# Kernel optimization log

Hardware: AMD Instinct MI355X
Metric: run time of the kernel (lower is better)

## Reference

```python
import jax, jax.numpy as jnp
import numpy as np

ATTN_MULT = 8.0
NEG_INF = float('-inf')

N, Q, S, D = 16, 2048, 2048, 64


def setup_inputs() -> dict:
    key = jax.random.key(0)
    kq, kk, kv, kp = jax.random.split(key, 4)
    return {
        "queries_nqd": jax.random.normal(kq, (N, Q, D), dtype=jnp.float32),
        "keys_nsd": jax.random.normal(kk, (N, S, D), dtype=jnp.float32),
        "values_nsv": jax.random.normal(kv, (N, S, D), dtype=jnp.float32),
        "prefix_len_n": jax.random.randint(kp, (N,), 0, S, dtype=jnp.int64 if jax.config.jax_enable_x64 else jnp.int32),
    }


def reference(queries_nqd, keys_nsd, values_nsv, prefix_len_n):
    # attention_type == 'block_diagonal', backend == 'torch', dropout p == 0
    n, q, d = queries_nqd.shape
    s = keys_nsd.shape[1]
    scale = ATTN_MULT / d
    # prefix-block mask: key position < prefix_len (broadcast over queries)
    block_mask_n1s = (jnp.arange(s)[None, None, :] < prefix_len_n[:, None, None])  # [n,1,s]
    diag_mask_qs = jnp.arange(q)[:, None] == jnp.arange(s)[None, :]                # [q,s]
    mask_nqs = block_mask_n1s | diag_mask_qs[None, :, :]                           # [n,q,s]
    scores_nqs = jnp.einsum('nqd,nsd->nqs', queries_nqd, keys_nsd) * scale
    scores_nqs = jnp.where(mask_nqs, scores_nqs, NEG_INF)
    probs_nqs = jax.nn.softmax(scores_nqs, axis=-1)
    return jnp.einsum('nqs,nsv->nqv', probs_nqs, values_nsv)
```

## Files before the change

kernel.cpp:

```cpp
#include <hip/hip_runtime.h>
#include <hip/hip_bf16.h>
#include <math.h>

#define NH 16
#define QL 2048
#define SL 2048
#define DD 64
#define BQ 128
#define NSPLIT 2
#define SPL 1024
#define NTILE 16
#define PSTR 72
#define QK_SCALE_LOG2E 0.1803368801111f

typedef __attribute__((ext_vector_type(8))) short short8;
typedef __attribute__((ext_vector_type(4))) float floatx4;
typedef __attribute__((ext_vector_type(4))) unsigned short ushort4v;
typedef __attribute__((ext_vector_type(8))) unsigned short ushort8v;

__device__ __forceinline__ unsigned short f2bf(float x) {
    unsigned u = __float_as_uint(x);
    u += 0x7FFFu + ((u >> 16) & 1u);
    return (unsigned short)(u >> 16);
}
__device__ __forceinline__ unsigned int f2bf2u(float x, float y) {
    __hip_bfloat162 h = __float22bfloat162_rn(make_float2(x, y));
    return *(unsigned int*)&h;
}
__device__ __forceinline__ float bf2f(unsigned short h) {
    return __uint_as_float((unsigned)h << 16);
}

__device__ __forceinline__ void gld16(const unsigned short* g, unsigned short* l) {
    __builtin_amdgcn_global_load_lds(
        (const __attribute__((address_space(1))) unsigned int*)g,
        (__attribute__((address_space(3))) unsigned int*)l, 16, 0, 0);
}

__global__ __launch_bounds__(512) void k_prep(
    const float* __restrict__ Kf, const float* __restrict__ Vf,
    unsigned short* __restrict__ Kb, unsigned short* __restrict__ Vtb)
{
    __shared__ unsigned short sT[64][PSTR];
    const int bx = (int)blockIdx.x, tid = (int)threadIdx.x;

    const int gidx = bx * 512 + tid;
    #pragma unroll
    for (int k = 0; k < 2; ++k) {
        int idx = gidx + k * (512 * 512);
        float4 v = ((const float4*)Kf)[idx];
        ushort4v h = { f2bf(v.x), f2bf(v.y), f2bf(v.z), f2bf(v.w) };
        *(ushort4v*)(Kb + (size_t)idx * 4) = h;
    }

    const int n = bx >> 5, s0 = (bx & 31) * 64;
    const float* vb = Vf + ((size_t)n * SL + s0) * DD;
    #pragma unroll
    for (int i = 0; i < 2; ++i) {
        int idx = tid + i * 512;
        int r = idx >> 4, c = (idx & 15) << 2;
        float4 v = *(const float4*)(vb + r * DD + c);
        sT[c + 0][r] = f2bf(v.x);
        sT[c + 1][r] = f2bf(v.y);
        sT[c + 2][r] = f2bf(v.z);
        sT[c + 3][r] = f2bf(v.w);
    }
    __syncthreads();
    const int d = tid >> 3, sg = tid & 7;
    unsigned short* out = Vtb + (size_t)n * DD * SL + (size_t)d * SL + s0 + sg * 8;
    ushort8v a;
    #pragma unroll
    for (int i = 0; i < 8; ++i) a[i] = sT[d][sg * 8 + i];
    *(ushort8v*)out = a;
}

__global__ __launch_bounds__(512, 6) void k_attn(
    const float* __restrict__ Qf, const unsigned short* __restrict__ Kb,
    const unsigned short* __restrict__ Vtb, const int* __restrict__ plen_g,
    unsigned short* __restrict__ Opb, float* __restrict__ Lp)
{
    __shared__ unsigned short sK[2][64 * 64];
    __shared__ unsigned short sVt[2][64 * 64];
    __shared__ unsigned short sP[8 * 16 * 64];

    const int flat = (int)blockIdx.x;
    const int sp   = flat >> 8;
    const int rb   = flat & 255;
    const int n    = (rb + sp) & (NH - 1);
    const int qt   = rb >> 4;
    const int q0   = qt * BQ;
    const int sbeg = sp * SPL;
    const int plen = plen_g[n];
    const bool hasdiag = (q0 >= sbeg) && (q0 < sbeg + SPL);
    if (!((sbeg < plen) || hasdiag)) return;

    const int tid  = (int)threadIdx.x;
    const int wave = tid >> 6, lane = tid & 63, quad = lane >> 4, l16 = lane & 15;

    int rem  = plen - sbeg;
    int base = (rem > 0) ? min((rem + 63) >> 6, NTILE) : 0;
    int td0 = -1, td1 = -1;
    if (hasdiag) {
        int d0 = (q0 - sbeg) >> 6;
        if (d0 >= base) td0 = d0;
        if (d0 + 1 >= base) td1 = d0 + 1;
    }
    const int total = base + (td0 >= 0) + (td1 >= 0);

    const int qrow  = wave * 16 + l16;
    const int qglob = q0 + qrow;
    const int pmask = (l16 & 7) * 8;

    const unsigned short* kh = Kb  + (size_t)n * SL * DD;
    const unsigned short* vh = Vtb + (size_t)n * DD * SL;

    const int srow = wave * 8 + (lane >> 3);
    const int scol = ((lane & 7) ^ (srow & 7)) * 8;

    auto tile_of = [&](int i) -> int {
        if (i < base) return i;
        if (i == base) return (td0 >= 0) ? td0 : td1;
        return td1;
    };

    {
        int t0 = tile_of(0);
        const unsigned short* kg = kh + (size_t)(sbeg + t0 * 64) * DD;
        const unsigned short* vg = vh + (sbeg + t0 * 64);
        gld16(kg + srow * DD + scol, sK[0] + wave * 512);
        gld16(vg + (size_t)srow * SL + scol, sVt[0] + wave * 512);
    }

    short8 bQ0, bQ1;
    {
        const float* qf = Qf + ((size_t)(n * QL + qglob)) * DD + quad * 8;
        float4 a0 = *(const float4*)(qf);
        float4 a1 = *(const float4*)(qf + 4);
        float4 c0 = *(const float4*)(qf + 32);
        float4 c1 = *(const float4*)(qf + 36);
        const float S = QK_SCALE_LOG2E;
        unsigned int u0[4] = {
            f2bf2u(a0.x * S, a0.y * S), f2bf2u(a0.z * S, a0.w * S),
            f2bf2u(a1.x * S, a1.y * S), f2bf2u(a1.z * S, a1.w * S) };
        unsigned int u1[4] = {
            f2bf2u(c0.x * S, c0.y * S), f2bf2u(c0.z * S, c0.w * S),
            f2bf2u(c1.x * S, c1.y * S), f2bf2u(c1.z * S, c1.w * S) };
        bQ0 = *(short8*)u0;
        bQ1 = *(short8*)u1;
    }

    floatx4 acc[4];
    #pragma unroll
    for (int dt = 0; dt < 4; ++dt) acc[dt] = (floatx4){0.f, 0.f, 0.f, 0.f};
    float lsum = 0.f;
    unsigned short* pw = sP + qrow * 64;

    for (int i = 0; i < total; ++i) {
        __syncthreads();

        if (i + 1 < total) {
            int tn = tile_of(i + 1);
            const unsigned short* kg = kh + (size_t)(sbeg + tn * 64) * DD;
            const unsigned short* vg = vh + (sbeg + tn * 64);
            gld16(kg + srow * DD + scol, sK[(i + 1) & 1] + wave * 512);
            gld16(vg + (size_t)srow * SL + scol, sVt[(i + 1) & 1] + wave * 512);
        }

        const unsigned short* sk = sK[i & 1];
        const unsigned short* sv = sVt[i & 1];
        const int t  = tile_of(i);
        const int s0 = sbeg + t * 64;

        floatx4 sf[4];
        #pragma unroll
        for (int st2 = 0; st2 < 4; ++st2) sf[st2] = (floatx4){0.f, 0.f, 0.f, 0.f};
        __builtin_amdgcn_s_setprio(1);
        #pragma unroll
        for (int st2 = 0; st2 < 4; ++st2) {
            int krow = st2 * 16 + l16;
            short8 aK0 = *(const short8*)(sk + krow * 64 + (((0 * 4 + quad) ^ (krow & 7)) * 8));
            short8 aK1 = *(const short8*)(sk + krow * 64 + (((1 * 4 + quad) ^ (krow & 7)) * 8));
            sf[st2] = __builtin_amdgcn_mfma_f32_16x16x32_bf16(aK0, bQ0, sf[st2], 0, 0, 0);
            sf[st2] = __builtin_amdgcn_mfma_f32_16x16x32_bf16(aK1, bQ1, sf[st2], 0, 0, 0);
        }
        __builtin_amdgcn_s_setprio(0);

        if (s0 + 64 <= plen) {
            #pragma unroll
            for (int st2 = 0; st2 < 4; ++st2) {
                float p0 = __builtin_amdgcn_exp2f(sf[st2][0]);
                float p1 = __builtin_amdgcn_exp2f(sf[st2][1]);
                float p2 = __builtin_amdgcn_exp2f(sf[st2][2]);
                float p3 = __builtin_amdgcn_exp2f(sf[st2][3]);
                lsum += (p0 + p1) + (p2 + p3);
                uint2 pk = { f2bf2u(p0, p1), f2bf2u(p2, p3) };
                *(uint2*)(pw + ((st2 * 16 + quad * 4) ^ pmask)) = pk;
            }
        } else {
            #pragma unroll
            for (int st2 = 0; st2 < 4; ++st2) {
                float p[4];
                #pragma unroll
                for (int r2 = 0; r2 < 4; ++r2) {
                    int s = s0 + st2 * 16 + quad * 4 + r2;
                    bool valid = (s < plen) || (s == qglob);
                    p[r2] = __builtin_amdgcn_exp2f(valid ? sf[st2][r2] : -INFINITY);
                    lsum += p[r2];
                }
                uint2 pk = { f2bf2u(p[0], p[1]), f2bf2u(p[2], p[3]) };
                *(uint2*)(pw + ((st2 * 16 + quad * 4) ^ pmask)) = pk;
            }
        }

        __builtin_amdgcn_s_setprio(1);
        #pragma unroll
        for (int ks = 0; ks < 2; ++ks) {
            short8 aP = *(const short8*)(pw + ((ks * 32 + quad * 8) ^ pmask));
            #pragma unroll
            for (int dt = 0; dt < 4; ++dt) {
                int vrow = dt * 16 + l16;
                short8 bV = *(const short8*)(sv + vrow * 64 + (((ks * 4 + quad) ^ (vrow & 7)) * 8));
                acc[dt] = __builtin_amdgcn_mfma_f32_16x16x32_bf16(aP, bV, acc[dt], 0, 0, 0);
            }
        }
        __builtin_amdgcn_s_setprio(0);
    }

    lsum += __shfl_xor(lsum, 16, 64);
    lsum += __shfl_xor(lsum, 32, 64);
    if (quad == 0)
        Lp[((size_t)sp * NH + n) * QL + q0 + qrow] = lsum;

    unsigned short* pws = sP + wave * 16 * 64;
    #pragma unroll
    for (int dt = 0; dt < 4; ++dt) {
        int chunk = dt * 2 + (l16 >> 3);
        #pragma unroll
        for (int r2 = 0; r2 < 4; ++r2) {
            int row = quad * 4 + r2;
            int sw = ((chunk ^ (row & 7)) * 8) + (l16 & 7);
            pws[row * 64 + sw] = f2bf(acc[dt][r2]);
        }
    }
    const size_t qbase = ((size_t)sp * NH + n) * QL + q0 + wave * 16;
    #pragma unroll
    for (int t2 = 0; t2 < 2; ++t2) {
        int row = t2 * 8 + (lane >> 3);
        int chunk = lane & 7;
        int sw = (chunk ^ (row & 7)) * 8;
        ushort8v val = *(const ushort8v*)(pws + row * 64 + sw);
        *(ushort8v*)(Opb + (qbase + row) * DD + chunk * 8) = val;
    }
}

__global__ __launch_bounds__(512) void k_combine(
    const unsigned short* __restrict__ Opb, const float* __restrict__ Lp,
    const int* __restrict__ plen_g, float* __restrict__ Og)
{
    const int idx = (int)(blockIdx.x * 512 + threadIdx.x);
    const int d8 = idx & 7;
    const int q  = (idx >> 3) & (QL - 1);
    const int n  = idx >> 14;
    const int plen = plen_g[n];
    const int spd = q >> 10;
    float s[8];
    #pragma unroll
    for (int j = 0; j < 8; ++j) s[j] = 0.f;
    float l = 0.f;
    #pragma unroll
    for (int sp = 0; sp < NSPLIT; ++sp) {
        if ((sp * SPL < plen) || (sp == spd)) {
            const unsigned short* ob = Opb + (((size_t)sp * NH + n) * QL + q) * DD + d8 * 8;
            ushort8v v = *(const ushort8v*)ob;
            #pragma unroll
            for (int j = 0; j < 8; ++j) s[j] += bf2f(v[j]);
            l += Lp[((size_t)sp * NH + n) * QL + q];
        }
    }
    const float inv = 1.0f / l;
    float4 o0 = { s[0] * inv, s[1] * inv, s[2] * inv, s[3] * inv };
    float4 o1 = { s[4] * inv, s[5] * inv, s[6] * inv, s[7] * inv };
    float* og = Og + ((size_t)n * QL + q) * DD + d8 * 8;
    *(float4*)og = o0;
    *(float4*)(og + 4) = o1;
}

extern "C" void kernel_launch(void* const* d_in, const int* in_sizes, int n_in,
                              void* d_out, int out_size, void* d_ws, size_t ws_size,
                              hipStream_t stream) {
    const float* Qf   = (const float*)d_in[0];
    const float* Kf   = (const float*)d_in[1];
    const float* Vf   = (const float*)d_in[2];
    const int*   plen = (const int*)d_in[3];
    float* Og = (float*)d_out;

    char* ws = (char*)d_ws;
    unsigned short* Kb  = (unsigned short*)(ws);
    unsigned short* Vtb = (unsigned short*)(ws + (4u << 20));
    unsigned short* Opb = (unsigned short*)(ws + (8u << 20));
    float*          Lp  = (float*)(ws + (16u << 20));

    k_prep<<<512, 512, 0, stream>>>(Kf, Vf, Kb, Vtb);
    k_attn<<<NSPLIT * 256, 512, 0, stream>>>(Qf, Kb, Vtb, plen, Opb, Lp);
    k_combine<<<512, 512, 0, stream>>>(Opb, Lp, plen, Og);
}
```

Measured before the change: 107.2 us.

## Interleave key tiles across splits and triple-buffer K/V loads with explicit waitcnt

The key sequence is now split between the two split-K blocks by tile parity (even tiles to one split, odd tiles to the other) instead of contiguous halves. This balances prefix work between the splits, since a short prefix previously loaded nearly all the work onto the first split. Each split also takes one of the two diagonal tiles, so both splits always produce output and the combine kernel drops its plen-dependent checks. The K/V shared-memory staging becomes a 3-deep ring with manual vmcnt waits and raw barriers, keeping two tiles in flight. The extra LDS this needs is why the occupancy hint drops from 6 to 4 blocks.

```diff
diff --git a/kernel.cpp b/kernel.cpp
--- a/kernel.cpp
+++ b/kernel.cpp
@@ -8,8 +8,6 @@
 #define DD 64
 #define BQ 128
 #define NSPLIT 2
-#define SPL 1024
-#define NTILE 16
 #define PSTR 72
 #define QK_SCALE_LOG2E 0.1803368801111f
 
@@ -74,13 +72,13 @@
     *(ushort8v*)out = a;
 }
 
-__global__ __launch_bounds__(512, 6) void k_attn(
+__global__ __launch_bounds__(512, 4) void k_attn(
     const float* __restrict__ Qf, const unsigned short* __restrict__ Kb,
     const unsigned short* __restrict__ Vtb, const int* __restrict__ plen_g,
     unsigned short* __restrict__ Opb, float* __restrict__ Lp)
 {
-    __shared__ unsigned short sK[2][64 * 64];
-    __shared__ unsigned short sVt[2][64 * 64];
+    __shared__ unsigned short sK[3][64 * 64];
+    __shared__ unsigned short sVt[3][64 * 64];
     __shared__ unsigned short sP[8 * 16 * 64];
 
     const int flat = (int)blockIdx.x;
@@ -89,23 +87,16 @@
     const int n    = (rb + sp) & (NH - 1);
     const int qt   = rb >> 4;
     const int q0   = qt * BQ;
-    const int sbeg = sp * SPL;
     const int plen = plen_g[n];
-    const bool hasdiag = (q0 >= sbeg) && (q0 < sbeg + SPL);
-    if (!((sbeg < plen) || hasdiag)) return;
 
     const int tid  = (int)threadIdx.x;
     const int wave = tid >> 6, lane = tid & 63, quad = lane >> 4, l16 = lane & 15;
 
-    int rem  = plen - sbeg;
-    int base = (rem > 0) ? min((rem + 63) >> 6, NTILE) : 0;
-    int td0 = -1, td1 = -1;
-    if (hasdiag) {
-        int d0 = (q0 - sbeg) >> 6;
-        if (d0 >= base) td0 = d0;
-        if (d0 + 1 >= base) td1 = d0 + 1;
-    }
-    const int total = base + (td0 >= 0) + (td1 >= 0);
+    const int ptiles = (plen + 63) >> 6;
+    const int d0     = q0 >> 6;
+    const int tdiag  = d0 + sp;
+    const int cnt_p  = (ptiles + 1 - sp) >> 1;
+    const int total  = cnt_p + (tdiag >= ptiles ? 1 : 0);
 
     const int qrow  = wave * 16 + l16;
     const int qglob = q0 + qrow;
@@ -118,18 +109,14 @@
     const int scol = ((lane & 7) ^ (srow & 7)) * 8;
 
     auto tile_of = [&](int i) -> int {
-        if (i < base) return i;
-        if (i == base) return (td0 >= 0) ? td0 : td1;
-        return td1;
+        return (i < cnt_p) ? (sp + (i << 1)) : tdiag;
     };
-
-    {
-        int t0 = tile_of(0);
-        const unsigned short* kg = kh + (size_t)(sbeg + t0 * 64) * DD;
-        const unsigned short* vg = vh + (sbeg + t0 * 64);
-        gld16(kg + srow * DD + scol, sK[0] + wave * 512);
-        gld16(vg + (size_t)srow * SL + scol, sVt[0] + wave * 512);
-    }
+    auto stage = [&](int t, int b) {
+        const unsigned short* kg = kh + ((size_t)t << 6) * DD;
+        const unsigned short* vg = vh + (t << 6);
+        gld16(kg + srow * DD + scol, sK[b] + wave * 512);
+        gld16(vg + (size_t)srow * SL + scol, sVt[b] + wave * 512);
+    };
 
     short8 bQ0, bQ1;
     {
@@ -149,27 +136,31 @@
         bQ1 = *(short8*)u1;
     }
 
+    stage(tile_of(0), 0);
+    if (total > 1) stage(tile_of(1), 1);
+
     floatx4 acc[4];
     #pragma unroll
     for (int dt = 0; dt < 4; ++dt) acc[dt] = (floatx4){0.f, 0.f, 0.f, 0.f};
     float lsum = 0.f;
     unsigned short* pw = sP + qrow * 64;
 
+    int bi = 0;
+    int bs = 2;
     for (int i = 0; i < total; ++i) {
-        __syncthreads();
-
-        if (i + 1 < total) {
-            int tn = tile_of(i + 1);
-            const unsigned short* kg = kh + (size_t)(sbeg + tn * 64) * DD;
-            const unsigned short* vg = vh + (sbeg + tn * 64);
-            gld16(kg + srow * DD + scol, sK[(i + 1) & 1] + wave * 512);
-            gld16(vg + (size_t)srow * SL + scol, sVt[(i + 1) & 1] + wave * 512);
-        }
-
-        const unsigned short* sk = sK[i & 1];
-        const unsigned short* sv = sVt[i & 1];
+        if (i + 2 <= total) {
+            asm volatile("s_waitcnt vmcnt(2) lgkmcnt(0)" ::: "memory");
+        } else {
+            asm volatile("s_waitcnt vmcnt(0) lgkmcnt(0)" ::: "memory");
+        }
+        __builtin_amdgcn_s_barrier();
+
+        if (i + 2 < total) stage(tile_of(i + 2), bs);
+
+        const unsigned short* sk = sK[bi];
+        const unsigned short* sv = sVt[bi];
         const int t  = tile_of(i);
-        const int s0 = sbeg + t * 64;
+        const int s0 = t << 6;
 
         floatx4 sf[4];
         #pragma unroll
@@ -224,6 +215,9 @@
             }
         }
         __builtin_amdgcn_s_setprio(0);
+
+        bi = (bi == 2) ? 0 : bi + 1;
+        bs = (bs == 2) ? 0 : bs + 1;
     }
 
     lsum += __shfl_xor(lsum, 16, 64);
@@ -255,27 +249,23 @@
 
 __global__ __launch_bounds__(512) void k_combine(
     const unsigned short* __restrict__ Opb, const float* __restrict__ Lp,
-    const int* __restrict__ plen_g, float* __restrict__ Og)
+    float* __restrict__ Og)
 {
     const int idx = (int)(blockIdx.x * 512 + threadIdx.x);
     const int d8 = idx & 7;
     const int q  = (idx >> 3) & (QL - 1);
     const int n  = idx >> 14;
-    const int plen = plen_g[n];
-    const int spd = q >> 10;
     float s[8];
     #pragma unroll
     for (int j = 0; j < 8; ++j) s[j] = 0.f;
     float l = 0.f;
     #pragma unroll
     for (int sp = 0; sp < NSPLIT; ++sp) {
-        if ((sp * SPL < plen) || (sp == spd)) {
-            const unsigned short* ob = Opb + (((size_t)sp * NH + n) * QL + q) * DD + d8 * 8;
-            ushort8v v = *(const ushort8v*)ob;
-            #pragma unroll
-            for (int j = 0; j < 8; ++j) s[j] += bf2f(v[j]);
-            l += Lp[((size_t)sp * NH + n) * QL + q];
-        }
+        const unsigned short* ob = Opb + (((size_t)sp * NH + n) * QL + q) * DD + d8 * 8;
+        ushort8v v = *(const ushort8v*)ob;
+        #pragma unroll
+        for (int j = 0; j < 8; ++j) s[j] += bf2f(v[j]);
+        l += Lp[((size_t)sp * NH + n) * QL + q];
     }
     const float inv = 1.0f / l;
     float4 o0 = { s[0] * inv, s[1] * inv, s[2] * inv, s[3] * inv };
@@ -302,5 +292,5 @@
 
     k_prep<<<512, 512, 0, stream>>>(Kf, Vf, Kb, Vtb);
     k_attn<<<NSPLIT * 256, 512, 0, stream>>>(Qf, Kb, Vtb, plen, Opb, Lp);
-    k_combine<<<512, 512, 0, stream>>>(Opb, Lp, plen, Og);
-}
+    k_combine<<<512, 512, 0, stream>>>(Opb, Lp, Og);
+}
```

Measured after the change: 104.4 us. 1.03x faster.
